# Performance work log

Measured on AMD Instinct MI355X. Metric: run time of the kernel, lower is better.

## Reference

```python
import jax, jax.numpy as jnp
import numpy as np

NT = 16          # nt_states
TS = 48          # t_states
T = NT + TS      # total states
B, N = 4, 24     # batch, sentence length
HUGE = 1.0e9


def setup_inputs():
    key = jax.random.key(0)
    k1, k2, k3 = jax.random.split(key, 3)
    unary_scores = jax.nn.log_softmax(jax.random.normal(k1, (B, N, T), jnp.float32), axis=-1)
    rule = jax.random.normal(k2, (B, NT, N, T, T, 2), jnp.float32)
    rule_scores = jax.nn.log_softmax(rule.reshape(B, NT, N, -1), axis=-1).reshape(B, NT, N, T, T, 2)
    root_scores = jax.nn.log_softmax(jax.random.normal(k3, (B, NT), jnp.float32), axis=-1)
    return {"unary_scores": unary_scores, "rule_scores": rule_scores, "root_scores": root_scores}


def _lse(x, axes):
    return jax.nn.logsumexp(x, axis=axes)


def _inside(unary_scores, rule_scores, root_scores):
    Bv, Nv, Tt = unary_scores.shape
    nt = rule_scores.shape[1]
    dt = unary_scores.dtype
    R = jnp.moveaxis(rule_scores, 5, 0)            # (D, B, Tparent, H, TL, TR)

    # beta[b,l,r,t,h]: headed inside chart; betau[b,l,r,t]: head-summed chart
    beta = jnp.full((Bv, Nv + 1, Nv + 1, Tt, Nv), -HUGE, dt)
    betau = jnp.full((Bv, Nv + 1, Nv + 1, Tt), -HUGE, dt)

    # width-1 spans: only terminal states (word_span_slice = nt:T, nt_emission=False)
    ks = np.arange(Nv)
    st = np.arange(nt, Tt)
    beta = beta.at[:, ks[:, None], ks[:, None] + 1, st[None, :], ks[:, None]].set(0.0)
    betau = betau.at[:, ks[:, None], ks[:, None] + 1, st[None, :]].set(
        unary_scores[:, ks[:, None], st[None, :]])

    nts = np.arange(nt)
    for W in range(2, Nv + 1):
        L = Nv - W + 1
        ls = np.arange(L)
        rs = ls + W
        hidx = ls[:, None] + np.arange(W)          # (L, W) absolute head positions

        def width_body(beta, betau, R, unary_scores, W=W, ls=ls, rs=rs, hidx=hidx):
            def chartH(la, ra, s0, s1):            # (B, L, S, W)
                x = beta[:, la, ra, s0:s1, :]
                return jnp.take_along_axis(x, hidx[None, :, None, :], axis=3)

            def chartU(la, ra, s0, s1):            # (B, L, S)
                return betau[:, la, ra, s0:s1]

            def rwin(d, a0, a1, c0, c1):           # (B, L, nt, W, A, C)
                r = R[d][:, :, hidx, a0:a1, c0:c1]
                return jnp.transpose(r, (0, 2, 1, 3, 4, 5))

            def comb(xH, yU, xU, yH, z0, z1):
                # D=0: head from left child; D=1: head from right child.
                # logsumexp over TL, TR and both directions -> (B, L, nt, W)
                left = (jnp.transpose(xH, (0, 1, 3, 2))[:, :, None, :, :, None]
                        + yU[:, :, None, None, None, :] + z0)
                right = (xU[:, :, None, None, :, None]
                         + jnp.transpose(yH, (0, 1, 3, 2))[:, :, None, :, None, :] + z1)
                return jnp.logaddexp(_lse(left, (-2, -1)), _lse(right, (-2, -1)))

            c0, c1 = (nt, Tt) if W == 2 else (0, nt)
            # split at l+1: left child is a single terminal
            tmp = comb(chartH(ls, ls + 1, nt, Tt), chartU(ls + 1, rs, c0, c1),
                       chartU(ls, ls + 1, nt, Tt), chartH(ls + 1, rs, c0, c1),
                       rwin(0, nt, Tt, c0, c1), rwin(1, nt, Tt, c0, c1))
            if W >= 3:
                # split at r-1: right child is a single terminal
                tmp = jnp.logaddexp(tmp, comb(
                    chartH(ls, rs - 1, 0, nt), chartU(rs - 1, rs, nt, Tt),
                    chartU(ls, rs - 1, 0, nt), chartH(rs - 1, rs, nt, Tt),
                    rwin(0, 0, nt, nt, Tt), rwin(1, 0, nt, nt, Tt)))
            if W >= 4:
                # interior splits: both children are nonterminal spans
                z0 = rwin(0, 0, nt, 0, nt)
                z1 = rwin(1, 0, nt, 0, nt)
                for wl in range(2, W - 1):
                    s = ls + wl
                    tmp = jnp.logaddexp(tmp, comb(
                        chartH(ls, s, 0, nt), chartU(s, rs, 0, nt),
                        chartU(ls, s, 0, nt), chartH(s, rs, 0, nt), z0, z1))
            # add head-word emission under the parent NT; sum heads for betau
            uw = jnp.transpose(unary_scores[:, hidx, :nt], (0, 1, 3, 2))  # (B,L,nt,W)
            return tmp, _lse(tmp + uw, -1)

        tmp, tmpu = jax.checkpoint(width_body)(beta, betau, R, unary_scores)
        beta = beta.at[:, ls[:, None, None], rs[:, None, None],
                       nts[None, :, None], hidx[:, None, :]].set(tmp)
        betau = betau.at[:, ls[:, None], rs[:, None], nts[None, :]].set(tmpu)

    return jax.nn.logsumexp(betau[:, 0, Nv, :nt] + root_scores, axis=-1)  # log Z, (B,)


_inside_jit = jax.jit(_inside)


def reference(unary_scores, rule_scores, root_scores):
    return _inside_jit(unary_scores, rule_scores, root_scores)
```

## Files before the change

### kernel.cpp

```cpp
#include <hip/hip_runtime.h>
#include <cstddef>

#define Bv 4
#define Nv 24
#define NTv 16
#define Tv 64
#define NP 25
#define NEGF (-1e30f)

typedef __attribute__((ext_vector_type(8))) short short8v;
typedef __attribute__((ext_vector_type(4))) float f32x4;
union FragU { unsigned u[4]; short8v s; };

#define BETAA_OFF 0
#define BETAU_OFF 960000
#define RNT_OFF   1120000
#define T0_OFF    1906432
#define T1_OFF    2496256
#define T0L_OFF   3086080
#define T1R_OFF   3110656
#define D0_OFF    3135232
#define D1_OFF    3136768
#define EU_OFF    3138304
#define CELLF_OFF 3142912
#define WS_NEED   3145412

__device__ __forceinline__ void publish(float* p, float v) {
  __hip_atomic_store(p, v, __ATOMIC_RELAXED, __HIP_MEMORY_SCOPE_AGENT);
}

__device__ __forceinline__ unsigned packbf2(float lo, float hi) {
  unsigned bl = __float_as_uint(lo), bh = __float_as_uint(hi);
  bl = (bl + 0x7FFFu + ((bl >> 16) & 1u)) >> 16;
  bh = (bh + 0x7FFFu + ((bh >> 16) & 1u)) >> 16;
  return (bh << 16) | bl;
}

__global__ void init_kernel(const float* __restrict__ unary, float* __restrict__ betau,
                            float* __restrict__ Eu, int* __restrict__ cellF) {
  int t = blockIdx.x * blockDim.x + threadIdx.x;
  if (t < Bv * NP * NP) cellF[t] = 0;
  if (t >= Bv * Nv * 48) return;
  int i = t % 48, kk = (t / 48) % Nv, b = t / (48 * Nv);
  float u = unary[(size_t)(b * Nv + kk) * Tv + 16 + i];
  betau[((size_t)(b * NP + kk) * NP + (kk + 1)) * Tv + 16 + i] = u;
  Eu[(size_t)(b * Nv + kk) * 48 + i] = __expf(u);
}

__global__ __launch_bounds__(256) void prep_kernel(
    const float* __restrict__ rule, const float* __restrict__ Eu,
    unsigned* __restrict__ RNTh, float* __restrict__ T0, float* __restrict__ T1,
    float* __restrict__ T0L, float* __restrict__ T1R,
    float* __restrict__ D0, float* __restrict__ D1) {
  const int h = blockIdx.x, A = blockIdx.y, b = blockIdx.z;
  const int t = threadIdx.x;
  __shared__ float er0[64 * 65];
  __shared__ float er1[64 * 65];
  __shared__ float E[24 * 48];
  __shared__ float red[256];

  for (int i = t; i < 24 * 48; i += 256) E[i] = Eu[(size_t)b * (24 * 48) + i];
  const float* rb = rule + (size_t)((b * NTv + A) * Nv + h) * 8192;
#pragma unroll
  for (int i = 0; i < 8; ++i) {
    int lin = i * 1024 + t * 4;
    float4 v = *(const float4*)(rb + lin);
    int sL = lin >> 7, rem = (lin & 127) >> 1;
    er0[sL * 65 + rem] = __expf(v.x);
    er1[sL * 65 + rem] = __expf(v.y);
    er0[sL * 65 + rem + 1] = __expf(v.z);
    er1[sL * 65 + rem + 1] = __expf(v.w);
  }
  __syncthreads();
  {
    unsigned* dst0 = RNTh + (((size_t)(b * 2 + 0) * Nv + h) * NTv + A) * 128;
    unsigned* dst1 = RNTh + (((size_t)(b * 2 + 1) * Nv + h) * NTv + A) * 128;
    if (t < 128) {
      int sL = t >> 3, sRp = t & 7;
      dst0[t] = packbf2(er0[sL * 65 + 2 * sRp], er0[sL * 65 + 2 * sRp + 1]);
    } else {
      int t2 = t - 128;
      int sL = t2 >> 3, sRp = t2 & 7;
      dst1[t2] = packbf2(er1[sL * 65 + 2 * sRp], er1[sL * 65 + 2 * sRp + 1]);
    }
  }
  for (int o = t; o < 384; o += 256) {
    int p = o >> 4, sL = o & 15;
    const float* Ep = E + p * 48;
    const float* r0 = er0 + sL * 65 + 16;
    float acc = 0.f;
#pragma unroll 8
    for (int j = 0; j < 48; ++j) acc += Ep[j] * r0[j];
    T0[(((size_t)(b * Nv + h) * Nv + p) * NTv + sL) * NTv + A] = acc;
  }
  for (int o = t; o < 384; o += 256) {
    int p = o >> 4, sR = o & 15;
    const float* Ep = E + p * 48;
    float acc = 0.f;
#pragma unroll 8
    for (int i = 0; i < 48; ++i) acc += Ep[i] * er1[(16 + i) * 65 + sR];
    T1[(((size_t)(b * Nv + h) * Nv + p) * NTv + sR) * NTv + A] = acc;
  }
  if (t < 16) {
    float acc = 0.f;
    for (int i = 0; i < 48; ++i) acc += er0[(16 + i) * 65 + t];
    T0L[((size_t)(b * Nv + h) * NTv + t) * NTv + A] = acc;
  } else if (t < 32) {
    int sL = t - 16;
    float acc = 0.f;
    for (int j = 0; j < 48; ++j) acc += er1[sL * 65 + 16 + j];
    T1R[((size_t)(b * Nv + h) * NTv + sL) * NTv + A] = acc;
  }
  float acc0 = 0.f, acc1 = 0.f;
  const int hp = (h + 1 < 24) ? h + 1 : 0, hm = (h >= 1) ? h - 1 : 0;
  for (int e = t; e < 2304; e += 256) {
    int i = e / 48, j = e % 48;
    float r0 = er0[(16 + i) * 65 + 16 + j];
    float r1 = er1[(16 + i) * 65 + 16 + j];
    acc0 += E[hp * 48 + j] * r0;
    acc1 += E[hm * 48 + i] * r1;
  }
  red[t] = acc0;
  __syncthreads();
  if (t < 64) {
    float s = red[t] + red[t + 64] + red[t + 128] + red[t + 192];
#pragma unroll
    for (int off = 32; off; off >>= 1) s += __shfl_xor(s, off, 64);
    if (t == 0 && h <= 22) D0[((size_t)b * Nv + h) * NTv + A] = s;
  }
  __syncthreads();
  red[t] = acc1;
  __syncthreads();
  if (t < 64) {
    float s = red[t] + red[t + 64] + red[t + 128] + red[t + 192];
#pragma unroll
    for (int off = 32; off; off >>= 1) s += __shfl_xor(s, off, 64);
    if (t == 0 && h >= 1) D1[((size_t)b * Nv + (h - 1)) * NTv + A] = s;
  }
}

__device__ __forceinline__ void edge_dot(float v0, float v1, float v2, float v3,
                                         const float* Tb, float& sh, float& S) {
  float mx = fmaxf(fmaxf(v0, v1), fmaxf(v2, v3));
  mx = fmaxf(mx, __shfl_xor(mx, 1, 64));
  mx = fmaxf(mx, __shfl_xor(mx, 2, 64));
  float dot = __expf(v0 - mx) * Tb[0] + __expf(v1 - mx) * Tb[16] +
              __expf(v2 - mx) * Tb[32] + __expf(v3 - mx) * Tb[48];
  dot += __shfl_xor(dot, 1, 64);
  dot += __shfl_xor(dot, 2, 64);
  sh = mx;
  S = dot;
}

__global__ __launch_bounds__(768) void width_all_kernel(
    const float* __restrict__ unary, float* __restrict__ betaA, float* __restrict__ betau,
    const unsigned* __restrict__ RNTh, const float* __restrict__ T0, const float* __restrict__ T1,
    const float* __restrict__ T0L, const float* __restrict__ T1R,
    const float* __restrict__ D0, const float* __restrict__ D1,
    const float* __restrict__ root, float* __restrict__ out, int* __restrict__ cellF) {
  const int rr = blockIdx.x, b = blockIdx.y;
  const int r = rr + 2;
  const int tid = threadIdx.x;
  int* flagb = cellF + b * (NP * NP);

  __shared__ float chartC[23][384];
  __shared__ float buC[23][16];
  __shared__ float U0[24 * 256], U1[24 * 256];
  __shared__ float pM[2 * 24 * 16], pS[2 * 24 * 16];
  __shared__ float sTmp[16 * 24];
  __shared__ float uC[24][16];

  if (tid < 384) uC[tid >> 4][tid & 15] =
      unary[(size_t)(b * Nv + (tid >> 4)) * Tv + (tid & 15)];

  const int wv = tid >> 6, lane = tid & 63;
  const int sym = lane & 15;
  const int mBlk = (lane >> 4) * 8;

  for (int i = 0; i <= r - 2; ++i) {
    const int l = r - 2 - i;
    const int W = r - l;

    if (W >= 3) {
      if (tid < W - 3) {
        const int m = l + 2 + tid;
        while (__hip_atomic_load(&flagb[l * NP + m], __ATOMIC_RELAXED,
                                 __HIP_MEMORY_SCOPE_AGENT) == 0)
          __builtin_amdgcn_s_sleep(1);
      }
      __syncthreads();
    }

    float Gp[4];
#pragma unroll
    for (int pi = 0; pi < 4; ++pi) {
      const int p = wv + 12 * pi;
      if (p < 2 * W) {
        const int hh = p >> 1, d = p & 1, hcol = l + hh;
        int mst, cnt;
        if (d) { mst = l + 2; cnt = min(l + hh, r - 2) - mst + 1; }
        else   { mst = max(l + hh + 1, l + 2); cnt = (r - 2) - mst + 1; }
        if (cnt < 0) cnt = 0;
        float* Ua = (d ? U1 : U0) + hh * 256;
        if (cnt == 0) {
#pragma unroll
          for (int reg = 0; reg < 4; ++reg)
            Ua[((lane >> 4) * 4 + reg) * 16 + sym] = 0.f;
          Gp[pi] = -2e30f;
        } else {
          float Lv[8], Rv[8];
          if (d) {
            const size_t lb = ((size_t)(b * NP + l) * NP + mst) * Tv + sym;
#pragma unroll
            for (int j = 0; j < 8; ++j) {
              int mi = mBlk + j;
              Lv[j] = (mi < cnt) ? betau[lb + (size_t)mi * Tv] : NEGF;
              Rv[j] = (mi < cnt) ? chartC[mst + mi][hcol * 16 + sym] : NEGF;
            }
          } else {
            const size_t lb = ((size_t)(b * NP + l) * NP + mst) * 384 + hcol * 16 + sym;
#pragma unroll
            for (int j = 0; j < 8; ++j) {
              int mi = mBlk + j;
              Lv[j] = (mi < cnt) ? betaA[lb + (size_t)mi * 384] : NEGF;
              Rv[j] = (mi < cnt) ? buC[mst + mi][sym] : NEGF;
            }
          }
          float mxL = NEGF, mxR = NEGF;
#pragma unroll
          for (int j = 0; j < 8; ++j) { mxL = fmaxf(mxL, Lv[j]); mxR = fmaxf(mxR, Rv[j]); }
#pragma unroll
          for (int off = 1; off < 64; off <<= 1) {
            mxL = fmaxf(mxL, __shfl_xor(mxL, off, 64));
            mxR = fmaxf(mxR, __shfl_xor(mxR, off, 64));
          }
          FragU fa, fb;
#pragma unroll
          for (int jj = 0; jj < 4; ++jj) {
            int m0i = mBlk + 2 * jj, m1i = m0i + 1;
            float e0 = (m0i < cnt) ? __expf(Lv[2 * jj] - mxL) : 0.f;
            float e1 = (m1i < cnt) ? __expf(Lv[2 * jj + 1] - mxL) : 0.f;
            fa.u[jj] = packbf2(e0, e1);
            float f0 = (m0i < cnt) ? __expf(Rv[2 * jj] - mxR) : 0.f;
            float f1 = (m1i < cnt) ? __expf(Rv[2 * jj + 1] - mxR) : 0.f;
            fb.u[jj] = packbf2(f0, f1);
          }
          f32x4 z = {0.f, 0.f, 0.f, 0.f};
          f32x4 dU = __builtin_amdgcn_mfma_f32_16x16x32_bf16(fa.s, fb.s, z, 0, 0, 0);
#pragma unroll
          for (int reg = 0; reg < 4; ++reg)
            Ua[((lane >> 4) * 4 + reg) * 16 + sym] = dU[reg];
          Gp[pi] = mxL + mxR;
        }
      }
    }

    if (W >= 3) {
      while (__hip_atomic_load(&flagb[l * NP + (r - 1)], __ATOMIC_RELAXED,
                               __HIP_MEMORY_SCOPE_AGENT) == 0)
        __builtin_amdgcn_s_sleep(1);
    }

#pragma unroll
    for (int pi = 0; pi < 4; ++pi) {
      const int p = wv + 12 * pi;
      if (p < 2 * W) {
        const int hh = p >> 1, d = p & 1, h = l + hh;
        const float* Ua = (d ? U1 : U0) + hh * 256;
        const unsigned* Rb = RNTh + (((size_t)(b * 2 + d) * Nv + h) * NTv + sym) * 128;
        f32x4 acc4 = {0.f, 0.f, 0.f, 0.f};
#pragma unroll
        for (int kk = 0; kk < 8; ++kk) {
          uint4 ar = *(const uint4*)(Rb + kk * 16 + (lane >> 4) * 4);
          FragU fa, fb;
          fa.u[0] = ar.x; fa.u[1] = ar.y; fa.u[2] = ar.z; fa.u[3] = ar.w;
          if (sym == 0) {
            const float* up = Ua + kk * 32 + mBlk;
#pragma unroll
            for (int jj = 0; jj < 4; ++jj) fb.u[jj] = packbf2(up[2 * jj], up[2 * jj + 1]);
          } else {
            fb.u[0] = 0; fb.u[1] = 0; fb.u[2] = 0; fb.u[3] = 0;
          }
          acc4 = __builtin_amdgcn_mfma_f32_16x16x32_bf16(fa.s, fb.s, acc4, 0, 0, 0);
        }
        const int A = lane >> 2, q = lane & 3;
        const int src = (A >> 2) << 4;
        float c0 = __shfl(acc4[0], src, 64);
        float c1 = __shfl(acc4[1], src, 64);
        float c2 = __shfl(acc4[2], src, 64);
        float c3 = __shfl(acc4[3], src, 64);
        const int sel = A & 3;
        float acc = (sel == 0) ? c0 : (sel == 1) ? c1 : (sel == 2) ? c2 : c3;
        float Mi = Gp[pi];
        float sh2 = NEGF, S2 = 0.f, sh3 = NEGF, S3 = 0.f;
        if (W >= 3) {
          if (d == 0) {
            if (hh < W - 1) {
              const float* Tb = T0 + (((size_t)(b * Nv + h) * Nv + (r - 1)) * NTv + 4 * q) * NTv + A;
              float4 e4 = *(const float4*)(betaA +
                  ((size_t)(b * NP + l) * NP + (r - 1)) * 384 + (size_t)h * 16 + 4 * q);
              edge_dot(e4.x, e4.y, e4.z, e4.w, Tb, sh2, S2);
            }
            if (hh == 0) {
              const float* Tb = T0L + ((size_t)(b * Nv + l) * NTv + 4 * q) * NTv + A;
              const float* u4 = &buC[l + 1][4 * q];
              edge_dot(u4[0], u4[1], u4[2], u4[3], Tb, sh3, S3);
            }
          } else {
            if (hh >= 1) {
              const float* Tb = T1 + (((size_t)(b * Nv + h) * Nv + l) * NTv + 4 * q) * NTv + A;
              const float* e4 = &chartC[l + 1][h * 16 + 4 * q];
              edge_dot(e4[0], e4[1], e4[2], e4[3], Tb, sh2, S2);
            }
            if (hh == W - 1) {
              const float* Tb = T1R + ((size_t)(b * Nv + (r - 1)) * NTv + 4 * q) * NTv + A;
              float4 u4 = *(const float4*)(betau +
                  ((size_t)(b * NP + l) * NP + (r - 1)) * Tv + 4 * q);
              edge_dot(u4.x, u4.y, u4.z, u4.w, Tb, sh3, S3);
            }
          }
        } else {
          if (d == 0 && hh == 0) { sh2 = 0.f; S2 = D0[((size_t)b * Nv + l) * NTv + A]; }
          if (d == 1 && hh == 1) { sh2 = 0.f; S2 = D1[((size_t)b * Nv + l) * NTv + A]; }
        }
        float Mf = fmaxf(Mi, fmaxf(sh2, sh3));
        float Sf = acc * __expf(Mi - Mf) + S2 * __expf(sh2 - Mf) + S3 * __expf(sh3 - Mf);
        if (q == 0) {
          pM[(d * 24 + hh) * 16 + A] = Mf;
          pS[(d * 24 + hh) * 16 + A] = Sf;
        }
      }
    }
    __syncthreads();

    if (tid < 384) {
      int A2 = tid & 15, hh = tid >> 4;
      if (hh < W) {
        float M0 = pM[(0 * 24 + hh) * 16 + A2], S0 = pS[(0 * 24 + hh) * 16 + A2];
        float M1 = pM[(1 * 24 + hh) * 16 + A2], S1 = pS[(1 * 24 + hh) * 16 + A2];
        float nm = fmaxf(M0, M1);
        float s = S0 * __expf(M0 - nm) + S1 * __expf(M1 - nm);
        float val = nm + __logf(s);
        publish(&betaA[((size_t)(b * NP + l) * NP + r) * 384 + (l + hh) * 16 + A2], val);
        chartC[l][(l + hh) * 16 + A2] = val;
        sTmp[A2 * 24 + hh] = val + uC[l + hh][A2];
      }
    }
    __syncthreads();
    if (tid < 64) {
      const int A2 = tid & 15, g4 = tid >> 4;
      float mx = NEGF;
      for (int x = g4; x < W; x += 4) mx = fmaxf(mx, sTmp[A2 * 24 + x]);
      mx = fmaxf(mx, __shfl_xor(mx, 16, 64));
      mx = fmaxf(mx, __shfl_xor(mx, 32, 64));
      float s = 0.f;
      for (int x = g4; x < W; x += 4) s += __expf(sTmp[A2 * 24 + x] - mx);
      s += __shfl_xor(s, 16, 64);
      s += __shfl_xor(s, 32, 64);
      if (g4 == 0) {
        float val = mx + __logf(s);
        publish(&betau[((size_t)(b * NP + l) * NP + r) * Tv + A2], val);
        buC[l][A2] = val;
      }
    }
    if (tid == 0) {
      asm volatile("s_waitcnt vmcnt(0)" ::: "memory");
      __hip_atomic_store(&flagb[l * NP + r], 1, __ATOMIC_RELAXED,
                         __HIP_MEMORY_SCOPE_AGENT);
    }
  }

  if (rr == 22) {
    __syncthreads();
    if (tid == 0) {
      float vals[NTv];
      float mx = NEGF;
#pragma unroll
      for (int A = 0; A < NTv; ++A) {
        float v = buC[0][A] + root[b * NTv + A];
        vals[A] = v;
        mx = fmaxf(mx, v);
      }
      float s = 0.f;
#pragma unroll
      for (int A = 0; A < NTv; ++A) s += __expf(vals[A] - mx);
      out[b] = mx + __logf(s);
    }
  }
}

__global__ __launch_bounds__(768) void width_kernel_fb(
    const float* __restrict__ unary, const float* __restrict__ rule,
    float* __restrict__ betaA, float* __restrict__ betau, int W) {
  const int l = blockIdx.x, b = blockIdx.y;
  const int r = l + W;
  const int tid = threadIdx.x;
  const int sub = tid & 1;
  const int pid = tid >> 1;
  const int A = pid & 15;
  const int hh = pid >> 4;
  const int h = l + hh;
  const bool act = (hh < W);
  const int sA = tid & 15, sH = tid >> 4;

  __shared__ float sER0[48], sEL1[48];
  __shared__ float sCL0[16 * 24], sCR1[16 * 24];
  __shared__ float sMaxL0[24], sMaxR1[24];
  __shared__ float sShR0, sShL1;
  __shared__ float sTmp[16 * 24];

  float runM = NEGF, runS = 0.f;
  for (int m = l + 1; m < r; ++m) {
    const int wl = m - l, wr = r - m;
    if (tid < 64) {
      const int n = (wr == 1) ? 48 : 16, s0 = (wr == 1) ? 16 : 0;
      float v = (tid < n) ? betau[(size_t)((b * NP + m) * NP + r) * Tv + s0 + tid] : NEGF;
      float mx = v;
#pragma unroll
      for (int off = 32; off; off >>= 1) mx = fmaxf(mx, __shfl_xor(mx, off, 64));
      if (tid == 0) sShR0 = mx;
      if (tid < n) sER0[tid] = v - mx;
    } else if (tid < 128) {
      const int j = tid - 64;
      const int n = (wl == 1) ? 48 : 16, s0 = (wl == 1) ? 16 : 0;
      float v = (j < n) ? betau[(size_t)((b * NP + l) * NP + m) * Tv + s0 + j] : NEGF;
      float mx = v;
#pragma unroll
      for (int off = 32; off; off >>= 1) mx = fmaxf(mx, __shfl_xor(mx, off, 64));
      if (j == 0) sShL1 = mx;
      if (j < n) sEL1[j] = v - mx;
    }
    if (tid < 384) {
      if (wl > 1 && sH < wl) {
        float v = betaA[(size_t)((b * NP + l) * NP + m) * 384 + sA * Nv + (l + sH)];
        float mx = v;
#pragma unroll
        for (int off = 8; off; off >>= 1) mx = fmaxf(mx, __shfl_xor(mx, off, 16));
        if (sA == 0) sMaxL0[sH] = mx;
        sCL0[sA * Nv + sH] = v - mx;
      }
      if (wr > 1 && sH >= wl && sH < W) {
        float v = betaA[(size_t)((b * NP + m) * NP + r) * 384 + sA * Nv + (l + sH)];
        float mx = v;
#pragma unroll
        for (int off = 8; off; off >>= 1) mx = fmaxf(mx, __shfl_xor(mx, off, 16));
        if (sA == 0) sMaxR1[sH] = mx;
        sCR1[sA * Nv + sH] = v - mx;
      }
    }
    __syncthreads();
    if (act) {
      if (hh < wl && (wl > 1 || hh == 0)) {
        const int nL = (wl == 1) ? 48 : 16, sL0 = (wl == 1) ? 16 : 0;
        const int nR = (wr == 1) ? 48 : 16, sR0 = (wr == 1) ? 16 : 0;
        const float shift = ((wl == 1) ? 0.f : sMaxL0[hh]) + sShR0;
        float part = 0.f;
        const float* rb = rule + (size_t)(((b * NTv + A) * Nv + h) * Tv) * Tv * 2;
        for (int i = sub; i < nL; i += 2) {
          const float cl = (wl == 1) ? 0.f : sCL0[i * Nv + hh];
          const float* rp = rb + (size_t)(sL0 + i) * Tv * 2 + sR0 * 2;
#pragma unroll 8
          for (int j = 0; j < nR; ++j) part += __expf(cl + sER0[j] + rp[j * 2]);
        }
        float nm = fmaxf(runM, shift);
        runS = runS * __expf(runM - nm) + part * __expf(shift - nm);
        runM = nm;
      }
      if (hh >= wl && (wr > 1 || hh == W - 1)) {
        const int nL = (wl == 1) ? 48 : 16, sL0 = (wl == 1) ? 16 : 0;
        const int nR = (wr == 1) ? 48 : 16, sR0 = (wr == 1) ? 16 : 0;
        const float shift = sShL1 + ((wr == 1) ? 0.f : sMaxR1[hh]);
        float part = 0.f;
        const float* rb = rule + (size_t)(((b * NTv + A) * Nv + h) * Tv) * Tv * 2 + 1;
        for (int i = sub; i < nL; i += 2) {
          const float el = sEL1[i];
          const float* rp = rb + (size_t)(sL0 + i) * Tv * 2 + sR0 * 2;
#pragma unroll 8
          for (int j = 0; j < nR; ++j) {
            const float cr = (wr == 1) ? 0.f : sCR1[j * Nv + hh];
            part += __expf(el + cr + rp[j * 2]);
          }
        }
        float nm = fmaxf(runM, shift);
        runS = runS * __expf(runM - nm) + part * __expf(shift - nm);
        runM = nm;
      }
    }
    __syncthreads();
  }
  if (act) {
    float om = __shfl_xor(runM, 1, 64);
    float os = __shfl_xor(runS, 1, 64);
    float nm = fmaxf(runM, om);
    float s = runS * __expf(runM - nm) + os * __expf(om - nm);
    if (sub == 0) {
      float val = nm + __logf(s);
      betaA[(size_t)((b * NP + l) * NP + r) * 384 + A * Nv + h] = val;
      sTmp[A * Nv + hh] = val + unary[(b * Nv + h) * Tv + A];
    }
  }
  __syncthreads();
  if (tid < 16) {
    float mx = NEGF;
    for (int x = 0; x < W; ++x) mx = fmaxf(mx, sTmp[tid * Nv + x]);
    float s = 0.f;
    for (int x = 0; x < W; ++x) s += __expf(sTmp[tid * Nv + x] - mx);
    betau[(size_t)((b * NP + l) * NP + r) * Tv + tid] = mx + __logf(s);
  }
}

__global__ void final_kernel(const float* __restrict__ betau, const float* __restrict__ root,
                             float* __restrict__ out) {
  int b = threadIdx.x;
  if (b < Bv) {
    float vals[NTv];
    float mx = NEGF;
#pragma unroll
    for (int A = 0; A < NTv; ++A) {
      float v = betau[(size_t)((b * NP + 0) * NP + Nv) * Tv + A] + root[b * NTv + A];
      vals[A] = v;
      mx = fmaxf(mx, v);
    }
    float s = 0.f;
#pragma unroll
    for (int A = 0; A < NTv; ++A) s += __expf(vals[A] - mx);
    out[b] = mx + __logf(s);
  }
}

extern "C" void kernel_launch(void* const* d_in, const int* in_sizes, int n_in,
                              void* d_out, int out_size, void* d_ws, size_t ws_size,
                              hipStream_t stream) {
  (void)in_sizes; (void)n_in; (void)out_size;
  const float* unary = (const float*)d_in[0];
  const float* rule  = (const float*)d_in[1];
  const float* root  = (const float*)d_in[2];
  float* out = (float*)d_out;
  float* ws = (float*)d_ws;
  float* betaA = ws + BETAA_OFF;
  float* betau = ws + BETAU_OFF;
  const bool fast = ws_size >= (size_t)WS_NEED * sizeof(float);

  if (fast) {
    unsigned* RNTh = (unsigned*)(ws + RNT_OFF);
    float* T0  = ws + T0_OFF;
    float* T1  = ws + T1_OFF;
    float* T0L = ws + T0L_OFF;
    float* T1R = ws + T1R_OFF;
    float* D0  = ws + D0_OFF;
    float* D1  = ws + D1_OFF;
    float* Eu  = ws + EU_OFF;
    int* cellF = (int*)(ws + CELLF_OFF);
    init_kernel<<<(Bv * Nv * 48 + 255) / 256, 256, 0, stream>>>(unary, betau, Eu, cellF);
    prep_kernel<<<dim3(24, 16, 4), 256, 0, stream>>>(rule, Eu, RNTh, T0, T1, T0L, T1R, D0, D1);
    void* args[] = {(void*)&unary, (void*)&betaA, (void*)&betau, (void*)&RNTh,
                    (void*)&T0, (void*)&T1, (void*)&T0L, (void*)&T1R,
                    (void*)&D0, (void*)&D1, (void*)&root, (void*)&out, (void*)&cellF};
    hipLaunchCooperativeKernel((const void*)width_all_kernel, dim3(Nv - 1, Bv), dim3(768),
                               args, 0, stream);
  } else {
    float* Eu = ws + BETAU_OFF + 160000;
    int* prog = (int*)(ws + BETAU_OFF + 160000 + 4608);
    init_kernel<<<(Bv * Nv * 48 + 255) / 256, 256, 0, stream>>>(unary, betau, Eu, prog);
    for (int W = 2; W <= Nv; ++W) {
      dim3 grid(Nv - W + 1, Bv);
      width_kernel_fb<<<grid, 768, 0, stream>>>(unary, rule, betaA, betau, W);
    }
    final_kernel<<<1, 64, 0, stream>>>(betau, root, out);
  }
}
```

Measured before the change: 396.9 us.

## Replace per-cell flag wait with sentinel-based data polling on chart entries

Drops the per-cell flag spin-wait and instead polls the needed chart values directly, treating a NaN sentinel as not yet written. The init kernel now fills the whole betaA and betau charts with the sentinel, using a much larger grid. The aim is to let each wave start as soon as its own inputs land rather than waiting on a whole-cell flag. In exchange it adds a sizable init fill and relaxed atomic loads per element, and correctness depends on producers never writing the sentinel bit pattern and on memory ordering across the four loads.

```diff
diff --git a/kernel.cpp b/kernel.cpp
--- a/kernel.cpp
+++ b/kernel.cpp
@@ -7,6 +7,7 @@
 #define Tv 64
 #define NP 25
 #define NEGF (-1e30f)
+#define SENTU 0x7FC00001u
 
 typedef __attribute__((ext_vector_type(8))) short short8v;
 typedef __attribute__((ext_vector_type(4))) float f32x4;
@@ -36,15 +37,38 @@
   return (bh << 16) | bl;
 }
 
+__device__ __forceinline__ float4 poll4(const float* p) {
+  float4 v;
+  for (;;) {
+    v.x = __hip_atomic_load(p + 0, __ATOMIC_RELAXED, __HIP_MEMORY_SCOPE_AGENT);
+    v.y = __hip_atomic_load(p + 1, __ATOMIC_RELAXED, __HIP_MEMORY_SCOPE_AGENT);
+    v.z = __hip_atomic_load(p + 2, __ATOMIC_RELAXED, __HIP_MEMORY_SCOPE_AGENT);
+    v.w = __hip_atomic_load(p + 3, __ATOMIC_RELAXED, __HIP_MEMORY_SCOPE_AGENT);
+    if (__float_as_uint(v.x) != SENTU && __float_as_uint(v.y) != SENTU &&
+        __float_as_uint(v.z) != SENTU && __float_as_uint(v.w) != SENTU)
+      return v;
+    __builtin_amdgcn_s_sleep(1);
+  }
+}
+
 __global__ void init_kernel(const float* __restrict__ unary, float* __restrict__ betau,
-                            float* __restrict__ Eu, int* __restrict__ cellF) {
-  int t = blockIdx.x * blockDim.x + threadIdx.x;
-  if (t < Bv * NP * NP) cellF[t] = 0;
-  if (t >= Bv * Nv * 48) return;
-  int i = t % 48, kk = (t / 48) % Nv, b = t / (48 * Nv);
-  float u = unary[(size_t)(b * Nv + kk) * Tv + 16 + i];
-  betau[((size_t)(b * NP + kk) * NP + (kk + 1)) * Tv + 16 + i] = u;
-  Eu[(size_t)(b * Nv + kk) * 48 + i] = __expf(u);
+                            float* __restrict__ Eu, int* __restrict__ cellF,
+                            float* __restrict__ betaA) {
+  const int t0 = blockIdx.x * blockDim.x + threadIdx.x;
+  const int stride = gridDim.x * blockDim.x;
+  const float SENTF = __uint_as_float(SENTU);
+  for (int t = t0; t < Bv * NP * NP * 384; t += stride) betaA[t] = SENTF;
+  for (int t = t0; t < Bv * NP * NP * Tv; t += stride) {
+    int rl = (t / Tv) % NP, ll = (t / (Tv * NP)) % NP;
+    if (rl - ll != 1) betau[t] = SENTF;
+  }
+  if (t0 < Bv * NP * NP) cellF[t0] = 0;
+  if (t0 < Bv * Nv * 48) {
+    int i = t0 % 48, kk = (t0 / 48) % Nv, b = t0 / (48 * Nv);
+    float u = unary[(size_t)(b * Nv + kk) * Tv + 16 + i];
+    betau[((size_t)(b * NP + kk) * NP + (kk + 1)) * Tv + 16 + i] = u;
+    Eu[(size_t)(b * Nv + kk) * 48 + i] = __expf(u);
+  }
 }
 
 __global__ __launch_bounds__(256) void prep_kernel(
@@ -253,12 +277,6 @@
           Gp[pi] = mxL + mxR;
         }
       }
-    }
-
-    if (W >= 3) {
-      while (__hip_atomic_load(&flagb[l * NP + (r - 1)], __ATOMIC_RELAXED,
-                               __HIP_MEMORY_SCOPE_AGENT) == 0)
-        __builtin_amdgcn_s_sleep(1);
     }
 
 #pragma unroll
@@ -297,7 +315,7 @@
           if (d == 0) {
             if (hh < W - 1) {
               const float* Tb = T0 + (((size_t)(b * Nv + h) * Nv + (r - 1)) * NTv + 4 * q) * NTv + A;
-              float4 e4 = *(const float4*)(betaA +
+              float4 e4 = poll4(betaA +
                   ((size_t)(b * NP + l) * NP + (r - 1)) * 384 + (size_t)h * 16 + 4 * q);
               edge_dot(e4.x, e4.y, e4.z, e4.w, Tb, sh2, S2);
             }
@@ -314,7 +332,7 @@
             }
             if (hh == W - 1) {
               const float* Tb = T1R + ((size_t)(b * Nv + (r - 1)) * NTv + 4 * q) * NTv + A;
-              float4 u4 = *(const float4*)(betau +
+              float4 u4 = poll4(betau +
                   ((size_t)(b * NP + l) * NP + (r - 1)) * Tv + 4 * q);
               edge_dot(u4.x, u4.y, u4.z, u4.w, Tb, sh3, S3);
             }
@@ -551,17 +569,17 @@
     float* D1  = ws + D1_OFF;
     float* Eu  = ws + EU_OFF;
     int* cellF = (int*)(ws + CELLF_OFF);
-    init_kernel<<<(Bv * Nv * 48 + 255) / 256, 256, 0, stream>>>(unary, betau, Eu, cellF);
+    init_kernel<<<3750, 256, 0, stream>>>(unary, betau, Eu, cellF, betaA);
     prep_kernel<<<dim3(24, 16, 4), 256, 0, stream>>>(rule, Eu, RNTh, T0, T1, T0L, T1R, D0, D1);
     void* args[] = {(void*)&unary, (void*)&betaA, (void*)&betau, (void*)&RNTh,
                     (void*)&T0, (void*)&T1, (void*)&T0L, (void*)&T1R,
                     (void*)&D0, (void*)&D1, (void*)&root, (void*)&out, (void*)&cellF};
-    hipLaunchCooperativeKernel((const void*)width_all_kernel, dim3(Nv - 1, Bv), dim3(768),
-                               args, 0, stream);
+    (void)hipLaunchCooperativeKernel((const void*)width_all_kernel, dim3(Nv - 1, Bv),
+                                     dim3(768), args, 0, stream);
   } else {
     float* Eu = ws + BETAU_OFF + 160000;
     int* prog = (int*)(ws + BETAU_OFF + 160000 + 4608);
-    init_kernel<<<(Bv * Nv * 48 + 255) / 256, 256, 0, stream>>>(unary, betau, Eu, prog);
+    init_kernel<<<3750, 256, 0, stream>>>(unary, betau, Eu, prog, betaA);
     for (int W = 2; W <= Nv; ++W) {
       dim3 grid(Nv - W + 1, Bv);
       width_kernel_fb<<<grid, 768, 0, stream>>>(unary, rule, betaA, betau, W);
```

Result: no change. 402.4 us (+1.4%).
